# Kernel optimization log

Hardware: AMD Instinct MI355X
Metric: run time of the kernel (lower is better)

## Reference

```python
import jax, jax.numpy as jnp
import numpy as np

N = 50000
E = 800000
IN_DIM = 16
OUT_DIM = 16
EDGE_IN = 16
HID = 32


def setup_inputs() -> dict:
    key = jax.random.key(0)
    ks = jax.random.split(key, 9)
    x = jax.random.normal(ks[0], (N, IN_DIM), dtype=jnp.float32)
    edge_index = jax.random.randint(ks[1], (2, E), 0, N, dtype=jnp.int64)
    edge_attr = jax.random.normal(ks[2], (E, EDGE_IN), dtype=jnp.float32)
    # edge MLP params: Linear(EDGE_IN, 32) -> ReLU -> Linear(32, IN*OUT)
    w1 = jax.random.normal(ks[3], (EDGE_IN, HID), dtype=jnp.float32) * (1.0 / np.sqrt(EDGE_IN))
    b1 = jnp.zeros((HID,), dtype=jnp.float32)
    w2 = jax.random.normal(ks[4], (HID, IN_DIM * OUT_DIM), dtype=jnp.float32) * (1.0 / np.sqrt(HID))
    b2 = jnp.zeros((IN_DIM * OUT_DIM,), dtype=jnp.float32)
    # NNConv root weight and bias (defaults root_weight=True, bias=True)
    root = jax.random.normal(ks[5], (IN_DIM, OUT_DIM), dtype=jnp.float32) * (1.0 / np.sqrt(IN_DIM))
    bias = jnp.zeros((OUT_DIM,), dtype=jnp.float32)
    return {"x": x, "edge_index": edge_index, "edge_attr": edge_attr,
            "w1": w1, "b1": b1, "w2": w2, "b2": b2, "root": root, "bias": bias}


def reference(x, edge_index, edge_attr, w1, b1, w2, b2, root, bias):
    src = edge_index[0]  # x_j gathered from source nodes
    dst = edge_index[1]  # scatter-mean into target nodes
    # edge MLP -> per-edge weight matrix [E, IN, OUT]
    h = jax.nn.relu(edge_attr @ w1 + b1)
    W = (h @ w2 + b2).reshape(-1, IN_DIM, OUT_DIM)
    # per-edge matvec: message_e = x[src_e] @ W_e  -> [E, OUT]
    msg = jnp.einsum('ei,eio->eo', x[src], W)
    # scatter-mean aggregate into N target nodes
    summed = jax.ops.segment_sum(msg, dst, num_segments=N)
    cnt = jax.ops.segment_sum(jnp.ones((msg.shape[0],), dtype=msg.dtype), dst, num_segments=N)
    aggr = summed / jnp.maximum(cnt, 1.0)[:, None]
    return aggr + x @ root + bias
```

## Files before the change

kernel.cpp:

```cpp
#include <hip/hip_runtime.h>
#include <hip/hip_bf16.h>
#include <hip/hip_fp16.h>


#define N_NODES 50000
#define N_EDGES 800000
#define IN_D    16
#define OUT_D   16
#define HID_D   32
#define KTILES  17
#define NBLK_E  (N_EDGES / 256)
#define NBLK_N  (N_NODES * OUT_D / 256)
#define BLOB_BYTES 20480
#define BLOB_W1    17408
#define BLOB_B1    19456

#define WS_SUM   20480
#define WS_DEG   3220480
#define WS_NEED  (3220480 + (size_t)N_NODES * 4)

typedef __attribute__((ext_vector_type(8))) _Float16 hfrag8;
typedef __attribute__((ext_vector_type(4))) float f32x4;

__device__ __forceinline__ void fma4(float a, const float4 w, float4& m) {
    m.x = fmaf(a, w.x, m.x);
    m.y = fmaf(a, w.y, m.y);
    m.z = fmaf(a, w.z, m.z);
    m.w = fmaf(a, w.w, m.w);
}
__device__ __forceinline__ int clampn(int v) {
    return v < 0 ? 0 : (v >= N_NODES ? N_NODES - 1 : v);
}
__device__ __forceinline__ void gload_lds16(const void* g, void* l) {
    __builtin_amdgcn_global_load_lds(
        (const __attribute__((address_space(1))) unsigned int*)g,
        (__attribute__((address_space(3))) unsigned int*)l,
        16, 0, 0);
}


__global__ __launch_bounds__(256) void setup_k(
    const float* __restrict__ w1,
    const float* __restrict__ b1,
    const float* __restrict__ w2,
    const float* __restrict__ b2,
    unsigned char* __restrict__ blob)
{
    const int t = threadIdx.x;
    __half* bp = reinterpret_cast<__half*>(blob);
    for (int r = t; r < KTILES * 32; r += 256) {
        const int tile = r >> 5, q = (r >> 3) & 3, j = r & 7;
        const int base = ((tile * 4 + q) * 16) * 8 + j;
        float vals[16];
        if (r < 512) {
            const float4* wr = reinterpret_cast<const float4*>(w2) + r * 4;
            float4 v0 = wr[0], v1 = wr[1], v2 = wr[2], v3 = wr[3];
            vals[0]=v0.x; vals[1]=v0.y; vals[2]=v0.z; vals[3]=v0.w;
            vals[4]=v1.x; vals[5]=v1.y; vals[6]=v1.z; vals[7]=v1.w;
            vals[8]=v2.x; vals[9]=v2.y; vals[10]=v2.z; vals[11]=v2.w;
            vals[12]=v3.x; vals[13]=v3.y; vals[14]=v3.z; vals[15]=v3.w;
        } else if (r < 528) {
            const float4* br = reinterpret_cast<const float4*>(b2) + (r - 512) * 4;
            float4 v0 = br[0], v1 = br[1], v2 = br[2], v3 = br[3];
            vals[0]=v0.x; vals[1]=v0.y; vals[2]=v0.z; vals[3]=v0.w;
            vals[4]=v1.x; vals[5]=v1.y; vals[6]=v1.z; vals[7]=v1.w;
            vals[8]=v2.x; vals[9]=v2.y; vals[10]=v2.z; vals[11]=v2.w;
            vals[12]=v3.x; vals[13]=v3.y; vals[14]=v3.z; vals[15]=v3.w;
        } else {
            #pragma unroll
            for (int o = 0; o < 16; ++o) vals[o] = 0.f;
        }
        #pragma unroll
        for (int o = 0; o < 16; ++o) bp[base + o * 8] = __float2half(vals[o]);
    }
    float* wf = reinterpret_cast<float*>(blob + BLOB_W1);
    wf[t]       = w1[t];
    wf[t + 256] = w1[t + 256];
    if (t < HID_D) reinterpret_cast<float*>(blob + BLOB_B1)[t] = b1[t];
}


__global__ __launch_bounds__(256) void edge_k(
    const float* __restrict__ x,
    const int*   __restrict__ ei,
    const float* __restrict__ ea,
    const unsigned char* __restrict__ gblob,
    int*   __restrict__ deg,
    float* __restrict__ sum)
{
    __shared__ alignas(16) unsigned char s_blob[BLOB_BYTES];
    __shared__ alignas(16) __half s_h2[4 * 64 * 32];

    const int t    = threadIdx.x;
    const int lane = t & 63;
    const int w    = t >> 6;
    const int e    = blockIdx.x * 256 + t;

    #pragma unroll
    for (int j = 0; j < 5; ++j) {
        const int ch = w + 4 * j;
        gload_lds16(gblob + ch * 1024 + lane * 16, s_blob + ch * 1024);
    }

    const hfrag8* s_B  = reinterpret_cast<const hfrag8*>(s_blob);
    const float4* s_w1 = reinterpret_cast<const float4*>(s_blob + BLOB_W1);
    const float4* s_b1 = reinterpret_cast<const float4*>(s_blob + BLOB_B1);

    const int q   = lane >> 4;
    const int n   = lane & 15;
    const int qh  = q >> 1;
    const int i0q = (q & 1) * 8;

    const int src = clampn(ei[e]);
    const int dst = clampn(ei[N_EDGES + e]);
    atomicAdd(&deg[dst], 1);

    float4 xpre[4][2];
    #pragma unroll
    for (int sub = 0; sub < 4; ++sub) {
        const int srcB = __shfl(src, sub * 16 + n, 64);
        const float4* xp = reinterpret_cast<const float4*>(x) + (size_t)srcB * 4 + (i0q >> 2);
        xpre[sub][0] = xp[0];
        xpre[sub][1] = xp[1];
    }
    float eav[IN_D];
    {
        const float4* eap = reinterpret_cast<const float4*>(ea) + (size_t)e * 4;
        float4 a0 = eap[0], a1 = eap[1], a2 = eap[2], a3 = eap[3];
        eav[0]=a0.x;  eav[1]=a0.y;  eav[2]=a0.z;  eav[3]=a0.w;
        eav[4]=a1.x;  eav[5]=a1.y;  eav[6]=a1.z;  eav[7]=a1.w;
        eav[8]=a2.x;  eav[9]=a2.y;  eav[10]=a2.z; eav[11]=a2.w;
        eav[12]=a3.x; eav[13]=a3.y; eav[14]=a3.z; eav[15]=a3.w;
    }

    __syncthreads();

    {
        float4 hv[HID_D / 4];
        #pragma unroll
        for (int j = 0; j < HID_D / 4; ++j) hv[j] = s_b1[j];
        #pragma unroll
        for (int i = 0; i < IN_D; ++i) {
            const float xi = eav[i];
            #pragma unroll
            for (int j = 0; j < HID_D / 4; ++j) fma4(xi, s_w1[i * (HID_D / 4) + j], hv[j]);
        }
        union { hfrag8 v[4]; __half h[32]; } hp;
        #pragma unroll
        for (int jj = 0; jj < 8; ++jj) {
            const int k0 = 4 * jj;
            hp.h[((k0 + 0) & 1) * 16 + ((k0 + 0) >> 1)] = __float2half(fmaxf(hv[jj].x, 0.f));
            hp.h[((k0 + 1) & 1) * 16 + ((k0 + 1) >> 1)] = __float2half(fmaxf(hv[jj].y, 0.f));
            hp.h[((k0 + 2) & 1) * 16 + ((k0 + 2) >> 1)] = __float2half(fmaxf(hv[jj].z, 0.f));
            hp.h[((k0 + 3) & 1) * 16 + ((k0 + 3) >> 1)] = __float2half(fmaxf(hv[jj].w, 0.f));
        }
        hfrag8* rowv = reinterpret_cast<hfrag8*>(s_h2 + (size_t)w * 2048 + lane * 32);
        const int swl = (lane >> 1) & 3;
        rowv[0 ^ swl] = hp.v[0];
        rowv[1 ^ swl] = hp.v[1];
        rowv[2 ^ swl] = hp.v[2];
        rowv[3 ^ swl] = hp.v[3];
    }
    asm volatile("s_waitcnt lgkmcnt(0)" ::: "memory");
    __builtin_amdgcn_wave_barrier();

    const __half* hbase = s_h2 + (size_t)w * 2048;
    #pragma unroll
    for (int sub = 0; sub < 4; ++sub) {
        const int posW = sub * 16 + n;
        __half2 xh[4];
        {
            float4 xa = xpre[sub][0], xb = xpre[sub][1];
            xh[0] = __float22half2_rn(make_float2(xa.x, xa.y));
            xh[1] = __float22half2_rn(make_float2(xa.z, xa.w));
            xh[2] = __float22half2_rn(make_float2(xb.x, xb.y));
            xh[3] = __float22half2_rn(make_float2(xb.z, xb.w));
        }
        union { hfrag8 v; __half h[8]; } hA, hB;
        {
            const hfrag8* rowv = reinterpret_cast<const hfrag8*>(hbase + posW * 32);
            const int swr = (posW >> 1) & 3;
            hA.v = rowv[(2 * qh + 0) ^ swr];
            hB.v = rowv[(2 * qh + 1) ^ swr];
        }
        f32x4 acc = {0.f, 0.f, 0.f, 0.f};
        #pragma unroll
        for (int tile = 0; tile < 16; ++tile) {
            const __half hs = (tile < 8) ? hA.h[tile] : hB.h[tile - 8];
            const __half2 hh = __half2half2(hs);
            union { hfrag8 v; __half2 h[4]; } a;
            a.h[0] = __hmul2(hh, xh[0]);
            a.h[1] = __hmul2(hh, xh[1]);
            a.h[2] = __hmul2(hh, xh[2]);
            a.h[3] = __hmul2(hh, xh[3]);
            acc = __builtin_amdgcn_mfma_f32_16x16x32_f16(a.v, s_B[tile * 64 + lane], acc, 0, 0, 0);
        }
        {
            union { hfrag8 v; __half2 h[4]; } a;
            if (qh == 0) { a.h[0]=xh[0]; a.h[1]=xh[1]; a.h[2]=xh[2]; a.h[3]=xh[3]; }
            else { hfrag8 z = {0,0,0,0,0,0,0,0}; a.v = z; }
            acc = __builtin_amdgcn_mfma_f32_16x16x32_f16(a.v, s_B[16 * 64 + lane], acc, 0, 0, 0);
        }
        #pragma unroll
        for (int r = 0; r < 4; ++r) {
            const int dstB = __shfl(dst, sub * 16 + q * 4 + r, 64);
            unsafeAtomicAdd(&sum[(size_t)dstB * 16 + n], acc[r]);
        }
    }
}


__global__ __launch_bounds__(256) void node_k(
    const float* __restrict__ x,
    const float* __restrict__ root,
    const float* __restrict__ bias,
    const float* __restrict__ sum,
    const int*   __restrict__ deg,
    float* __restrict__ out)
{
    __shared__ float s_root[IN_D * OUT_D];
    __shared__ float s_bias[OUT_D];
    const int t = threadIdx.x;
    s_root[t] = root[t];
    if (t < OUT_D) s_bias[t] = bias[t];
    __syncthreads();

    const int g = blockIdx.x * 256 + t;
    const int n = g >> 4;
    const int o = g & 15;

    const float s = sum[g];
    const int   d = deg[n];
    float mv = s * (1.0f / (float)(d > 1 ? d : 1)) + s_bias[o];

    float xs[IN_D];
    {
        const float4* xp = reinterpret_cast<const float4*>(x) + (size_t)n * 4;
        float4 b0 = xp[0], b1v = xp[1], b2v = xp[2], b3 = xp[3];
        xs[0]=b0.x;  xs[1]=b0.y;  xs[2]=b0.z;  xs[3]=b0.w;
        xs[4]=b1v.x; xs[5]=b1v.y; xs[6]=b1v.z; xs[7]=b1v.w;
        xs[8]=b2v.x; xs[9]=b2v.y; xs[10]=b2v.z; xs[11]=b2v.w;
        xs[12]=b3.x; xs[13]=b3.y; xs[14]=b3.z; xs[15]=b3.w;
    }
    #pragma unroll
    for (int i = 0; i < IN_D; ++i)
        mv = fmaf(xs[i], s_root[i * OUT_D + o], mv);

    out[g] = mv;
}

extern "C" void kernel_launch(void* const* d_in, const int* in_sizes, int n_in,
                              void* d_out, int out_size, void* d_ws, size_t ws_size,
                              hipStream_t stream) {
    const float* x    = (const float*)d_in[0];
    const int*   ei   = (const int*)  d_in[1];
    const float* ea   = (const float*)d_in[2];
    const float* w1   = (const float*)d_in[3];
    const float* b1   = (const float*)d_in[4];
    const float* w2   = (const float*)d_in[5];
    const float* b2   = (const float*)d_in[6];
    const float* root = (const float*)d_in[7];
    const float* bias = (const float*)d_in[8];
    float* out = (float*)d_out;

    unsigned char* ws   = (unsigned char*)d_ws;
    unsigned char* blob = ws;
    float* sum = (float*)(ws + WS_SUM);
    int*   deg = (int*)(ws + WS_DEG);

    hipMemsetAsync(ws + WS_SUM, 0, (size_t)N_NODES * 16 * 4 + (size_t)N_NODES * 4, stream);
    setup_k<<<1, 256, 0, stream>>>(w1, b1, w2, b2, blob);
    edge_k<<<NBLK_E, 256, 0, stream>>>(x, ei, ea, blob, deg, sum);
    node_k<<<NBLK_N, 256, 0, stream>>>(x, root, bias, sum, deg, out);
}
```

Measured before the change: 184.3 us.

## Shrink LDS staging and prefetch x one sub-tile ahead to raise occupancy

Each wave now stages only a 16-row slice of the hidden activations in LDS, with the lanes of each sub-tile writing their row just before it is consumed. LDS per block drops from about 36 KB to about 24 KB. The x gathers for all four sub-tiles are no longer loaded up front; instead the next sub-tile's gather is prefetched while the current one runs, which cuts register pressure. A launch-bounds hint of 6 blocks per CU is added so more waves can be resident. The cost is extra wave barriers and LDS waits per sub-tile, and less memory-level parallelism on the x gathers.

```diff
diff --git a/kernel.cpp b/kernel.cpp
--- a/kernel.cpp
+++ b/kernel.cpp
@@ -80,7 +80,7 @@
 }
 
 
-__global__ __launch_bounds__(256) void edge_k(
+__global__ __launch_bounds__(256, 6) void edge_k(
     const float* __restrict__ x,
     const int*   __restrict__ ei,
     const float* __restrict__ ea,
@@ -89,7 +89,7 @@
     float* __restrict__ sum)
 {
     __shared__ alignas(16) unsigned char s_blob[BLOB_BYTES];
-    __shared__ alignas(16) __half s_h2[4 * 64 * 32];
+    __shared__ alignas(16) __half s_h2[4 * 16 * 32];
 
     const int t    = threadIdx.x;
     const int lane = t & 63;
@@ -110,19 +110,12 @@
     const int n   = lane & 15;
     const int qh  = q >> 1;
     const int i0q = (q & 1) * 8;
+    const int swz = (lane >> 1) & 3;
 
     const int src = clampn(ei[e]);
     const int dst = clampn(ei[N_EDGES + e]);
     atomicAdd(&deg[dst], 1);
 
-    float4 xpre[4][2];
-    #pragma unroll
-    for (int sub = 0; sub < 4; ++sub) {
-        const int srcB = __shfl(src, sub * 16 + n, 64);
-        const float4* xp = reinterpret_cast<const float4*>(x) + (size_t)srcB * 4 + (i0q >> 2);
-        xpre[sub][0] = xp[0];
-        xpre[sub][1] = xp[1];
-    }
     float eav[IN_D];
     {
         const float4* eap = reinterpret_cast<const float4*>(ea) + (size_t)e * 4;
@@ -132,9 +125,16 @@
         eav[8]=a2.x;  eav[9]=a2.y;  eav[10]=a2.z; eav[11]=a2.w;
         eav[12]=a3.x; eav[13]=a3.y; eav[14]=a3.z; eav[15]=a3.w;
     }
+    float4 xn0, xn1;
+    {
+        const int srcB = __shfl(src, n, 64);
+        const float4* xp = reinterpret_cast<const float4*>(x) + (size_t)srcB * 4 + (i0q >> 2);
+        xn0 = xp[0]; xn1 = xp[1];
+    }
 
     __syncthreads();
 
+    union { hfrag8 v[4]; __half h[32]; } hp;
     {
         float4 hv[HID_D / 4];
         #pragma unroll
@@ -145,7 +145,6 @@
             #pragma unroll
             for (int j = 0; j < HID_D / 4; ++j) fma4(xi, s_w1[i * (HID_D / 4) + j], hv[j]);
         }
-        union { hfrag8 v[4]; __half h[32]; } hp;
         #pragma unroll
         for (int jj = 0; jj < 8; ++jj) {
             const int k0 = 4 * jj;
@@ -154,35 +153,42 @@
             hp.h[((k0 + 2) & 1) * 16 + ((k0 + 2) >> 1)] = __float2half(fmaxf(hv[jj].z, 0.f));
             hp.h[((k0 + 3) & 1) * 16 + ((k0 + 3) >> 1)] = __float2half(fmaxf(hv[jj].w, 0.f));
         }
-        hfrag8* rowv = reinterpret_cast<hfrag8*>(s_h2 + (size_t)w * 2048 + lane * 32);
-        const int swl = (lane >> 1) & 3;
-        rowv[0 ^ swl] = hp.v[0];
-        rowv[1 ^ swl] = hp.v[1];
-        rowv[2 ^ swl] = hp.v[2];
-        rowv[3 ^ swl] = hp.v[3];
-    }
-    asm volatile("s_waitcnt lgkmcnt(0)" ::: "memory");
-    __builtin_amdgcn_wave_barrier();
-
-    const __half* hbase = s_h2 + (size_t)w * 2048;
+    }
+
+    __half* hwav = reinterpret_cast<__half*>(s_h2) + w * 512;
+
     #pragma unroll
     for (int sub = 0; sub < 4; ++sub) {
-        const int posW = sub * 16 + n;
-        __half2 xh[4];
-        {
-            float4 xa = xpre[sub][0], xb = xpre[sub][1];
-            xh[0] = __float22half2_rn(make_float2(xa.x, xa.y));
-            xh[1] = __float22half2_rn(make_float2(xa.z, xa.w));
-            xh[2] = __float22half2_rn(make_float2(xb.x, xb.y));
-            xh[3] = __float22half2_rn(make_float2(xb.z, xb.w));
-        }
+        const float4 xa = xn0, xb = xn1;
+        if (sub < 3) {
+            const int srcB = __shfl(src, (sub + 1) * 16 + n, 64);
+            const float4* xp = reinterpret_cast<const float4*>(x) + (size_t)srcB * 4 + (i0q >> 2);
+            xn0 = xp[0]; xn1 = xp[1];
+        }
+        asm volatile("s_waitcnt lgkmcnt(0)" ::: "memory");
+        __builtin_amdgcn_wave_barrier();
+        if ((lane >> 4) == sub) {
+            hfrag8* rowv = reinterpret_cast<hfrag8*>(hwav + (lane & 15) * 32);
+            rowv[0 ^ swz] = hp.v[0];
+            rowv[1 ^ swz] = hp.v[1];
+            rowv[2 ^ swz] = hp.v[2];
+            rowv[3 ^ swz] = hp.v[3];
+        }
+        asm volatile("s_waitcnt lgkmcnt(0)" ::: "memory");
+        __builtin_amdgcn_wave_barrier();
+
         union { hfrag8 v; __half h[8]; } hA, hB;
         {
-            const hfrag8* rowv = reinterpret_cast<const hfrag8*>(hbase + posW * 32);
-            const int swr = (posW >> 1) & 3;
-            hA.v = rowv[(2 * qh + 0) ^ swr];
-            hB.v = rowv[(2 * qh + 1) ^ swr];
-        }
+            const hfrag8* rowv = reinterpret_cast<const hfrag8*>(hwav + n * 32);
+            hA.v = rowv[(2 * qh + 0) ^ swz];
+            hB.v = rowv[(2 * qh + 1) ^ swz];
+        }
+        __half2 xh[4];
+        xh[0] = __float22half2_rn(make_float2(xa.x, xa.y));
+        xh[1] = __float22half2_rn(make_float2(xa.z, xa.w));
+        xh[2] = __float22half2_rn(make_float2(xb.x, xb.y));
+        xh[3] = __float22half2_rn(make_float2(xb.z, xb.w));
+
         f32x4 acc = {0.f, 0.f, 0.f, 0.f};
         #pragma unroll
         for (int tile = 0; tile < 16; ++tile) {
```

Result: no change. 184.0 us (-0.2%).
